# Performance work log

Hardware: AMD Instinct MI355X
Metric: run time of the kernel (lower is better)

## Reference

```python
import jax, jax.numpy as jnp
import numpy as np

N = 100_000   # nodes
E = 3_200_000 # edges
G = 512       # graphs in batch
H = 64        # hidden dim
C = 7         # num classes


def setup_inputs() -> dict:
    key = jax.random.key(0)
    ks = jax.random.split(key, 8)
    x = jax.random.normal(ks[0], (N, 1), dtype=jnp.float32)
    edge_index = jax.random.randint(ks[1], (2, E), 0, N, dtype=jnp.int32)
    batch = jnp.sort(jax.random.randint(ks[2], (N,), 0, G, dtype=jnp.int32))
    W1 = jax.random.normal(ks[3], (1, H), dtype=jnp.float32) / np.sqrt(1.0)
    b1 = jnp.zeros((H,), jnp.float32)
    W2 = jax.random.normal(ks[4], (H, H), dtype=jnp.float32) / np.sqrt(H)
    b2 = jnp.zeros((H,), jnp.float32)
    fW1 = jax.random.normal(ks[5], (H, 32), dtype=jnp.float32) / np.sqrt(H)
    fb1 = jnp.zeros((32,), jnp.float32)
    fW2 = jax.random.normal(ks[6], (32, C), dtype=jnp.float32) / np.sqrt(32.0)
    fb2 = jnp.zeros((C,), jnp.float32)
    return {"x": x, "edge_index": edge_index, "batch": batch,
            "W1": W1, "b1": b1, "W2": W2, "b2": b2,
            "fW1": fW1, "fb1": fb1, "fW2": fW2, "fb2": fb2}


def reference(x, edge_index, batch, W1, b1, W2, b2, fW1, fb1, fW2, fb2):
    # GCNConv with self-loops and symmetric normalization (PyG defaults).
    src, dst = edge_index[0], edge_index[1]
    loop = jnp.arange(N, dtype=src.dtype)
    s = jnp.concatenate([src, loop])  # [E+N]
    d = jnp.concatenate([dst, loop])
    deg = jax.ops.segment_sum(jnp.ones(s.shape, jnp.float32), d, num_segments=N)
    dis = jnp.where(deg > 0, jax.lax.rsqrt(jnp.maximum(deg, 1.0)), 0.0)
    norm = dis[s] * dis[d]  # [E+N]

    def gcn(h, W, b):
        h = h @ W                                   # [N, out]
        msg = norm[:, None] * h[s]                  # gather + scale
        return jax.ops.segment_sum(msg, d, num_segments=N) + b

    # Dropout is identity in eval/reference mode.
    h = jax.nn.relu(gcn(x, W1, b1))
    h = jax.nn.relu(gcn(h, W2, b2))

    # global_mean_pool over graph assignment `batch`
    cnt = jax.ops.segment_sum(jnp.ones((N,), jnp.float32), batch, num_segments=G)
    pooled = jax.ops.segment_sum(h, batch, num_segments=G) / jnp.maximum(cnt, 1.0)[:, None]

    h = jax.nn.relu(pooled @ fW1 + fb1)
    return h @ fW2 + fb2  # [G, C] logits
```

## Files before the change

### kernel.cpp

```cpp
#include <hip/hip_runtime.h>

#define N_NODES 100000
#define N_EDGES 3200000
#define G_GRAPHS 512
#define HDIM 64
#define CBSH 11
#define CBN 2048
#define NCB ((N_NODES + CBN - 1) / CBN)
#define EPW 4096
#define NWG ((N_EDGES + EPW - 1) / EPW)
#define EPT (EPW / 256)
#define SPL 16
#define WPS ((NWG + SPL - 1) / SPL)
#define MAXROWS 25

__global__ __launch_bounds__(256) void kprep(const float* __restrict__ W1,
                                             const float* __restrict__ b1,
                                             const float* __restrict__ W2,
                                             float* __restrict__ dt, int* __restrict__ meta,
                                             float* __restrict__ pw1, float* __restrict__ pb1,
                                             int* __restrict__ pdidx,
                                             float* __restrict__ w2p, float* __restrict__ tabs) {
    __shared__ float ts[HDIM], srt[HDIM];
    __shared__ int isnew[HDIM], rr[HDIM], kpermS[HDIM], rankS[HDIM];
    __shared__ int ndS;
    int tid = threadIdx.x;
    if (tid < HDIM) {
        float w1 = W1[tid], bb = b1[tid];
        ts[tid] = (w1 != 0.f) ? (-bb / w1) : -1e30f;
    }
    __syncthreads();
    if (tid < HDIM) {
        float tj = ts[tid];
        int r = 0;
        for (int i = 0; i < HDIM; ++i) {
            float ti = ts[i];
            if (ti < tj || (ti == tj && i < tid)) r++;
        }
        rr[tid] = r;
        srt[r] = tj;
        kpermS[r] = tid;
    }
    __syncthreads();
    if (tid < HDIM) {
        int r = rr[tid];
        isnew[r] = (r == 0) || (srt[r] != srt[r - 1]);
    }
    __syncthreads();
    if (tid < HDIM) {
        int r = rr[tid];
        int didx = 0;
        for (int q = 0; q <= r; ++q) didx += isnew[q];
        didx -= 1;
        rankS[tid] = didx;
        if (blockIdx.x == 0 && isnew[r]) dt[didx] = srt[r];
    }
    if (tid == 0) {
        int nd = 0;
        for (int q = 0; q < HDIM; ++q) nd += isnew[q];
        ndS = nd;
        if (blockIdx.x == 0) {
            int nw = 0;
            for (int q = 0; q < HDIM; ++q) nw |= (b1[q] != 0.f) ? 1 : 0;
            meta[0] = nd; meta[1] = nw;
        }
    }
    __syncthreads();
    int nd = ndS;
    if (blockIdx.x == 0 && tid < HDIM) {
        int pj = kpermS[tid];
        pw1[tid] = W1[pj]; pb1[tid] = b1[pj]; pdidx[tid] = rankS[pj];
    }
    int i = blockIdx.x * 256 + tid;
    if (i < HDIM * HDIM) {
        int r = i >> 6, j = i & 63;
        w2p[i] = W2[kpermS[r] * HDIM + j];
    }
    if (nd <= 6 && i < (1 + 4 * nd) * HDIM) {
        int r = i >> 6, j = i & 63;
        float acc = 0.f;
        if (r == 0) {
            for (int jj = 0; jj < HDIM; ++jj)
                if (W1[jj] == 0.f) acc += fmaxf(b1[jj], 0.f) * W2[jj * HDIM + j];
        } else {
            int q = (r - 1) >> 2, c = (r - 1) & 3;
            for (int jj = 0; jj < HDIM; ++jj) {
                if (rankS[jj] != q) continue;
                float w1 = W1[jj], bb = b1[jj];
                float wr = W2[jj * HDIM + j];
                if      (c == 0 && w1 > 0.f) acc += w1 * wr;
                else if (c == 1 && w1 < 0.f) acc += w1 * wr;
                else if (c == 2 && w1 > 0.f) acc += bb * wr;
                else if (c == 3 && w1 < 0.f) acc += bb * wr;
            }
        }
        tabs[i] = acc;
    }
}

__global__ void kzero(int* __restrict__ deg, float* __restrict__ q,
                      float* __restrict__ pool, int* __restrict__ cnt,
                      float* __restrict__ histA, float* __restrict__ histW) {
    size_t tid = (size_t)blockIdx.x * blockDim.x + threadIdx.x;
    size_t stride = (size_t)gridDim.x * blockDim.x;
    for (size_t i = tid; i < N_NODES; i += stride) { deg[i] = 0; q[i] = 0.f; }
    for (size_t i = tid; i < G_GRAPHS * HDIM; i += stride) pool[i] = 0.f;
    for (size_t i = tid; i < G_GRAPHS; i += stride) cnt[i] = 0;
    size_t nh = (size_t)7 * N_NODES;
    for (size_t i = tid; i < nh; i += stride) { histA[i] = 0.f; histW[i] = 0.f; }
}

__global__ __launch_bounds__(256) void kB2(const int* __restrict__ src,
                                           const int* __restrict__ dst,
                                           unsigned* __restrict__ sorted,
                                           int* __restrict__ wgcnt,
                                           int* __restrict__ wgpre) {
    __shared__ int hist[NCB];
    __shared__ int basep[NCB];
    __shared__ unsigned sbuf[EPW];
    int tid = threadIdx.x;
    int w = blockIdx.x;
    int e0 = w * EPW;
    int ecnt = min(EPW, N_EDGES - e0);
    if (tid < NCB) hist[tid] = 0;
    __syncthreads();
    int dreg[EPT], sreg[EPT];
    const uint4* dst4 = reinterpret_cast<const uint4*>(dst + e0);
    const uint4* src4 = reinterpret_cast<const uint4*>(src + e0);
    #pragma unroll
    for (int t = 0; t < EPT / 4; ++t) {
        int v = t * 256 + tid;
        if (v * 4 < ecnt) {
            uint4 dv = dst4[v];
            uint4 sv = src4[v];
            int base = v * 4;
            int d0 = (int)dv.x, d1 = (int)dv.y, d2 = (int)dv.z, d3 = (int)dv.w;
            dreg[t*4+0] = (base+0 < ecnt) ? d0 : -1;
            dreg[t*4+1] = (base+1 < ecnt) ? d1 : -1;
            dreg[t*4+2] = (base+2 < ecnt) ? d2 : -1;
            dreg[t*4+3] = (base+3 < ecnt) ? d3 : -1;
            sreg[t*4+0] = (int)sv.x; sreg[t*4+1] = (int)sv.y;
            sreg[t*4+2] = (int)sv.z; sreg[t*4+3] = (int)sv.w;
            #pragma unroll
            for (int k = 0; k < 4; ++k)
                if (dreg[t*4+k] >= 0) atomicAdd(&hist[dreg[t*4+k] >> CBSH], 1);
        } else {
            dreg[t*4+0] = dreg[t*4+1] = dreg[t*4+2] = dreg[t*4+3] = -1;
        }
    }
    __syncthreads();
    if (tid < 64) {
        int h = (tid < NCB) ? hist[tid] : 0;
        int v = h;
        #pragma unroll
        for (int off = 1; off < 64; off <<= 1) {
            int uu = __shfl_up(v, off, 64);
            if (tid >= off) v += uu;
        }
        if (tid < NCB) {
            basep[tid] = v - h;
            wgcnt[w * NCB + tid] = h;
            wgpre[w * NCB + tid] = v - h;
        }
    }
    __syncthreads();
    #pragma unroll
    for (int t = 0; t < EPT; ++t) {
        int d = dreg[t];
        if (d >= 0) {
            int b = d >> CBSH;
            int pos = atomicAdd(&basep[b], 1);
            sbuf[pos] = ((unsigned)sreg[t] << CBSH) | (unsigned)(d & (CBN - 1));
        }
    }
    __syncthreads();
    uint4* out4 = reinterpret_cast<uint4*>(sorted + e0);
    const uint4* sb4 = reinterpret_cast<const uint4*>(sbuf);
    int nv4 = ecnt >> 2;
    for (int i = tid; i < nv4; i += 256) out4[i] = sb4[i];
    for (int i = (nv4 << 2) + tid; i < ecnt; i += 256) sorted[e0 + i] = sbuf[i];
}

#define FOR_RUNS(BODY)                                                        \
    {                                                                         \
        int wv = tid >> 6, ln = tid & 63;                                     \
        int w0 = sp * WPS, w1e = min(w0 + WPS, NWG);                          \
        for (int w = w0 + wv; w < w1e; w += 4) {                              \
            int st = w * EPW + wgpre[w * NCB + b];                            \
            int cb = wgcnt[w * NCB + b];                                      \
            for (int i = ln; i < cb; i += 64) { unsigned ww = sorted[st + i]; BODY } \
        }                                                                     \
    }

__global__ __launch_bounds__(256) void kdeg2(const unsigned* __restrict__ sorted,
                                             const int* __restrict__ wgcnt,
                                             const int* __restrict__ wgpre,
                                             int* __restrict__ deg) {
    __shared__ int dcnt[CBN];
    int b = blockIdx.x / SPL, sp = blockIdx.x % SPL, tid = threadIdx.x;
    for (int i = tid; i < CBN; i += 256) dcnt[i] = 0;
    __syncthreads();
    FOR_RUNS( atomicAdd(&dcnt[ww & (CBN - 1)], 1); )
    __syncthreads();
    int nb = b * CBN;
    for (int i = tid; i < CBN; i += 256) {
        int c = dcnt[i];
        if (c && nb + i < N_NODES) atomicAdd(&deg[nb + i], c);
    }
}

__global__ void k2_dis(const int* __restrict__ deg, const float* __restrict__ x,
                       float* __restrict__ dis, float* __restrict__ u) {
    int n = blockIdx.x * blockDim.x + threadIdx.x;
    if (n < N_NODES) {
        float d = rsqrtf((float)(deg[n] + 1));
        dis[n] = d;
        u[n] = d * x[n];
    }
}

__global__ __launch_bounds__(256) void kq3(const unsigned* __restrict__ sorted,
                                           const int* __restrict__ wgcnt,
                                           const int* __restrict__ wgpre,
                                           const float* __restrict__ u,
                                           float* __restrict__ q) {
    __shared__ float qL[CBN];
    int b = blockIdx.x / SPL, sp = blockIdx.x % SPL, tid = threadIdx.x;
    for (int i = tid; i < CBN; i += 256) qL[i] = 0.f;
    __syncthreads();
    FOR_RUNS( atomicAdd(&qL[ww & (CBN - 1)], u[ww >> CBSH]); )
    __syncthreads();
    int nb = b * CBN;
    for (int i = tid; i < CBN; i += 256) {
        float v = qL[i];
        if (v != 0.f && nb + i < N_NODES) atomicAdd(&q[nb + i], v);
    }
}

__global__ void k3b(const int* __restrict__ deg, const float* __restrict__ x,
                    const float* __restrict__ dis, const float* __restrict__ q,
                    float2* __restrict__ ad) {
    int n = blockIdx.x * blockDim.x + threadIdx.x;
    if (n < N_NODES) {
        float d = dis[n];
        ad[n] = make_float2(d * q[n] + x[n] / (float)(deg[n] + 1), d);
    }
}

template<int LO, int HI, int PLANES>
__global__ __launch_bounds__(256) void khist3t(const unsigned* __restrict__ sorted,
                                               const int* __restrict__ wgcnt,
                                               const int* __restrict__ wgpre,
                                               const float2* __restrict__ ad,
                                               const float* __restrict__ dt,
                                               const int* __restrict__ meta,
                                               float* __restrict__ histA,
                                               float* __restrict__ histW) {
    __shared__ float bA[PLANES * CBN];
    __shared__ float dtS[8];
    int nd = meta[0], needW = meta[1];
    if (nd < LO || nd > HI) return;
    int b = blockIdx.x / SPL, sp = blockIdx.x % SPL, tid = threadIdx.x;
    if (tid < 8) dtS[tid] = (tid < nd) ? dt[tid] : 3.4e38f;
    int nb = b * CBN;
    int nparts = 1 + (needW ? 1 : 0);
    for (int part = 0; part < nparts; ++part) {
        for (int i = tid; i < (nd + 1) * CBN; i += 256) bA[i] = 0.f;
        __syncthreads();
        FOR_RUNS(
            float2 t = ad[ww >> CBSH];
            float a = t.x;
            int k = 0;
            _Pragma("unroll")
            for (int qq = 0; qq < HI; ++qq) k += (dtS[qq] < a) ? 1 : 0;
            atomicAdd(&bA[k * CBN + (ww & (CBN - 1))], part ? t.y : t.y * a);
        )
        __syncthreads();
        float* H = part ? histW : histA;
        for (int k = 0; k <= nd; ++k)
            for (int i = tid; i < CBN; i += 256) {
                float v = bA[k * CBN + i];
                if (v != 0.f && nb + i < N_NODES)
                    atomicAdd(&H[(size_t)k * N_NODES + nb + i], v);
            }
        __syncthreads();
    }
}

__global__ __launch_bounds__(256) void knode(
        const float* __restrict__ histA, const float* __restrict__ histW,
        const int* __restrict__ meta, const float* __restrict__ dt,
        const float* __restrict__ tabs,
        const float* __restrict__ pw1, const float* __restrict__ pb1,
        const float* __restrict__ w2p,
        const float2* __restrict__ ad, const float* __restrict__ b2,
        const int* __restrict__ batch,
        const unsigned* __restrict__ sorted, const int* __restrict__ wgcnt,
        const int* __restrict__ wgpre,
        float* __restrict__ pool, int* __restrict__ cnt) {
    __shared__ float h2s[HDIM * 65];
    __shared__ float tabL[MAXROWS * HDIM];
    __shared__ float dtS[8];
    int tid = threadIdx.x;
    int nl = tid & 63, cg = tid >> 6;
    int n0 = blockIdx.x * 64;
    int nvalid = min(64, N_NODES - n0);
    int n = n0 + min(nl, nvalid - 1);
    int nd = meta[0], needW = meta[1];
    float2 adn = ad[n];
    float a = adn.x, d = adn.y;
    int c16 = cg * 16;

    if (nd <= 6) {
        int nrows = 1 + 4 * nd;
        for (int i = tid; i < nrows * HDIM; i += 256) tabL[i] = tabs[i];
        if (tid < nd) dtS[tid] = dt[tid];
        __syncthreads();
        float TA = 0.f, TW = 0.f;
        for (int bq = 0; bq <= nd; ++bq) {
            TA += histA[(size_t)bq * N_NODES + n];
            if (needW) TW += histW[(size_t)bq * N_NODES + n];
        }
        int k = 0;
        for (int q = 0; q < nd; ++q) k += (dtS[q] < a) ? 1 : 0;
        float z[16];
        #pragma unroll
        for (int t = 0; t < 16; ++t) z[t] = b2[c16 + t];
        float d2 = d * d;
        float cC = d * TW + d2;
        #pragma unroll
        for (int t = 0; t < 16; ++t) z[t] += cC * tabL[c16 + t];
        float run = 0.f, runW = 0.f;
        for (int q = 0; q < nd; ++q) {
            run += histA[(size_t)q * N_NODES + n];
            if (needW) runW += histW[(size_t)q * N_NODES + n];
            bool act = (q < k);
            float cWp = d * (TA - run) + (act ? d2 * a : 0.f);
            float cWm = d * run + (act ? 0.f : d2 * a);
            float cBp = d * (TW - runW) + (act ? d2 : 0.f);
            float cBm = d * runW + (act ? 0.f : d2);
            int base = (1 + 4 * q) * HDIM + c16;
            #pragma unroll
            for (int t = 0; t < 16; ++t)
                z[t] += cWp * tabL[base + t] + cWm * tabL[base + HDIM + t]
                      + cBp * tabL[base + 2 * HDIM + t] + cBm * tabL[base + 3 * HDIM + t];
        }
        #pragma unroll
        for (int t = 0; t < 16; ++t) h2s[nl * 65 + c16 + t] = fmaxf(z[t], 0.f);
    } else {
        float areg[HDIM];
        #pragma unroll
        for (int jj = 0; jj < HDIM; ++jj) areg[jj] = 0.f;
        int b = n >> CBSH;
        int myld = n & (CBN - 1);
        for (int w = 0; w < NWG; ++w) {
            int st = w * EPW + wgpre[w * NCB + b];
            int cb = wgcnt[w * NCB + b];
            for (int i = 0; i < cb; ++i) {
                unsigned ww = sorted[st + i];
                if ((int)(ww & (CBN - 1)) == myld) {
                    float2 t = ad[ww >> CBSH];
                    #pragma unroll
                    for (int jj = 0; jj < HDIM; ++jj)
                        areg[jj] += t.y * fmaxf(t.x * pw1[jj] + pb1[jj], 0.f);
                }
            }
        }
        #pragma unroll
        for (int jj = 0; jj < HDIM; ++jj)
            areg[jj] = d * areg[jj] + d * d * fmaxf(a * pw1[jj] + pb1[jj], 0.f);
        float z[16];
        #pragma unroll
        for (int t = 0; t < 16; ++t) z[t] = b2[c16 + t];
        for (int jj = 0; jj < HDIM; ++jj) {
            float av = areg[jj];
            #pragma unroll
            for (int t = 0; t < 16; ++t) z[t] += av * w2p[jj * HDIM + c16 + t];
        }
        #pragma unroll
        for (int t = 0; t < 16; ++t) h2s[nl * 65 + c16 + t] = fmaxf(z[t], 0.f);
    }

    __syncthreads();
    int i0 = cg * 16, i1 = min(i0 + 16, nvalid);
    float accP = 0.f; int gcur = -1, runC = 0;
    for (int i = i0; i < i1; ++i) {
        int g = batch[n0 + i];
        float v = h2s[i * 65 + nl];
        if (g != gcur) {
            if (gcur >= 0) {
                atomicAdd(&pool[(size_t)gcur * HDIM + nl], accP);
                if (nl == 0) atomicAdd(&cnt[gcur], runC);
            }
            gcur = g; accP = 0.f; runC = 0;
        }
        accP += v; ++runC;
    }
    if (gcur >= 0) {
        atomicAdd(&pool[(size_t)gcur * HDIM + nl], accP);
        if (nl == 0) atomicAdd(&cnt[gcur], runC);
    }
}

__global__ void k7_mlp(const float* __restrict__ pool, const int* __restrict__ cnt,
                       const float* __restrict__ fW1, const float* __restrict__ fb1,
                       const float* __restrict__ fW2, const float* __restrict__ fb2,
                       float* __restrict__ out) {
    __shared__ float p[HDIM];
    __shared__ float tt[32];
    int g = blockIdx.x;
    int tid = threadIdx.x;
    float c = fmaxf((float)cnt[g], 1.f);
    p[tid] = pool[g * HDIM + tid] / c;
    __syncthreads();
    if (tid < 32) {
        float acc = fb1[tid];
        #pragma unroll
        for (int j = 0; j < HDIM; ++j) acc += p[j] * fW1[j * 32 + tid];
        tt[tid] = fmaxf(acc, 0.f);
    }
    __syncthreads();
    if (tid < 7) {
        float acc = fb2[tid];
        #pragma unroll
        for (int i = 0; i < 32; ++i) acc += tt[i] * fW2[i * 7 + tid];
        out[g * 7 + tid] = acc;
    }
}

__global__ void kf1_deg(const int* __restrict__ dst, int* __restrict__ deg) {
    int e = blockIdx.x * blockDim.x + threadIdx.x;
    if (e < N_EDGES) atomicAdd(&deg[dst[e]], 1);
}
__global__ void kf2_dis(const int* __restrict__ deg, const float* __restrict__ x,
                        float* __restrict__ dis, float* __restrict__ agg1) {
    int n = blockIdx.x * blockDim.x + threadIdx.x;
    if (n < N_NODES) {
        float d = (float)(deg[n] + 1);
        dis[n] = rsqrtf(d);
        agg1[n] = x[n] / d;
    }
}
__global__ void kf3_agg1(const int* __restrict__ src, const int* __restrict__ dst,
                         const float* __restrict__ dis, const float* __restrict__ x,
                         float* __restrict__ agg1) {
    int e = blockIdx.x * blockDim.x + threadIdx.x;
    if (e < N_EDGES) {
        int s = src[e], d = dst[e];
        atomicAdd(&agg1[d], dis[s] * dis[d] * x[s]);
    }
}
__global__ void kf4_agg2init(const float* __restrict__ agg1, const float* __restrict__ dis,
                             const float* __restrict__ W1, const float* __restrict__ b1,
                             float* __restrict__ agg2) {
    int i = blockIdx.x * blockDim.x + threadIdx.x;
    if (i < N_NODES * HDIM) {
        int n = i >> 6, j = i & 63;
        float h = fmaxf(agg1[n] * W1[j] + b1[j], 0.f);
        float r = dis[n];
        agg2[i] = r * r * h;
    }
}
__global__ void kf5_edge(const int* __restrict__ src, const int* __restrict__ dst,
                         const float* __restrict__ dis, const float* __restrict__ agg1,
                         const float* __restrict__ W1, const float* __restrict__ b1,
                         float* __restrict__ agg2) {
    int t = blockIdx.x * blockDim.x + threadIdx.x;
    int e = t >> 6, j = t & 63;
    if (e < N_EDGES) {
        int s = src[e], d = dst[e];
        float w = dis[s] * dis[d];
        float h = fmaxf(agg1[s] * W1[j] + b1[j], 0.f);
        atomicAdd(&agg2[d * HDIM + j], w * h);
    }
}
__global__ void kf6_pool(const float* __restrict__ agg2, const float* __restrict__ W2,
                         const float* __restrict__ b2, const int* __restrict__ batch,
                         float* __restrict__ pool, int* __restrict__ cnt) {
    __shared__ float w2s[HDIM * HDIM];
    int tid = threadIdx.x;
    for (int i = tid; i < HDIM * HDIM; i += blockDim.x) w2s[i] = W2[i];
    __syncthreads();
    int lane = tid & 63, wid = tid >> 6;
    int nwaves = gridDim.x * 4;
    for (int n = blockIdx.x * 4 + wid; n < N_NODES; n += nwaves) {
        float av  = agg2[n * HDIM + lane];
        float acc = b2[lane];
        #pragma unroll
        for (int k = 0; k < HDIM; ++k)
            acc += __shfl(av, k, 64) * w2s[k * HDIM + lane];
        acc = fmaxf(acc, 0.f);
        int g = batch[n];
        atomicAdd(&pool[g * HDIM + lane], acc);
        if (lane == 0) atomicAdd(&cnt[g], 1);
    }
}

extern "C" void kernel_launch(void* const* d_in, const int* in_sizes, int n_in,
                              void* d_out, int out_size, void* d_ws, size_t ws_size,
                              hipStream_t stream) {
    const float* x    = (const float*)d_in[0];
    const int*   ei   = (const int*)  d_in[1];
    const int*   batch= (const int*)  d_in[2];
    const float* W1   = (const float*)d_in[3];
    const float* b1   = (const float*)d_in[4];
    const float* W2   = (const float*)d_in[5];
    const float* b2   = (const float*)d_in[6];
    const float* fW1  = (const float*)d_in[7];
    const float* fb1  = (const float*)d_in[8];
    const float* fW2  = (const float*)d_in[9];
    const float* fb2  = (const float*)d_in[10];
    const int* src = ei;
    const int* dst = ei + N_EDGES;
    float* out = (float*)d_out;

    size_t off = 0;
    auto take = [&](size_t bytes) { size_t o = off; off = (off + bytes + 255) & ~(size_t)255; return o; };
    char* base = (char*)d_ws;
    int*     deg   = (int*)     (base + take((size_t)N_NODES * 4));
    float*   pool  = (float*)   (base + take((size_t)G_GRAPHS * HDIM * 4));
    int*     cnt   = (int*)     (base + take((size_t)G_GRAPHS * 4));
    float*   dis   = (float*)   (base + take((size_t)N_NODES * 4));
    float*   u     = (float*)   (base + take((size_t)N_NODES * 4));
    float*   q     = (float*)   (base + take((size_t)N_NODES * 4));
    float2*  ad    = (float2*)  (base + take((size_t)N_NODES * 8));
    float*   dt    = (float*)   (base + take(HDIM * 4));
    int*     meta  = (int*)     (base + take(64));
    float*   pw1   = (float*)   (base + take(HDIM * 4));
    float*   pb1   = (float*)   (base + take(HDIM * 4));
    int*     pdidx = (int*)     (base + take(HDIM * 4));
    float*   w2p   = (float*)   (base + take(HDIM * HDIM * 4));
    float*   tabs  = (float*)   (base + take((size_t)MAXROWS * HDIM * 4));
    int*     wgcnt = (int*)     (base + take((size_t)NWG * NCB * 4));
    int*     wgpre = (int*)     (base + take((size_t)NWG * NCB * 4));
    size_t sorted_off = off;
    unsigned* sorted = (unsigned*)(base + take((size_t)N_EDGES * 4));
    float*   histA = (float*)   (base + take((size_t)7 * N_NODES * 4));
    float*   histW = (float*)   (base + take((size_t)7 * N_NODES * 4));
    size_t need_fast = off;

    if (ws_size >= need_fast) {
        kprep <<<16, 256, 0, stream>>>(W1, b1, W2, dt, meta, pw1, pb1, pdidx, w2p, tabs);
        kzero <<<1024, 256, 0, stream>>>(deg, q, pool, cnt, histA, histW);
        kB2   <<<NWG, 256, 0, stream>>>(src, dst, sorted, wgcnt, wgpre);
        kdeg2 <<<NCB * SPL, 256, 0, stream>>>(sorted, wgcnt, wgpre, deg);
        k2_dis<<<(N_NODES + 255) / 256, 256, 0, stream>>>(deg, x, dis, u);
        kq3   <<<NCB * SPL, 256, 0, stream>>>(sorted, wgcnt, wgpre, u, q);
        k3b   <<<(N_NODES + 255) / 256, 256, 0, stream>>>(deg, x, dis, q, ad);
        khist3t<0, 1, 2><<<NCB * SPL, 256, 0, stream>>>(sorted, wgcnt, wgpre, ad, dt, meta, histA, histW);
        khist3t<2, 6, 7><<<NCB * SPL, 256, 0, stream>>>(sorted, wgcnt, wgpre, ad, dt, meta, histA, histW);
        knode <<<(N_NODES + 63) / 64, 256, 0, stream>>>(histA, histW, meta, dt, tabs,
                                                        pw1, pb1, w2p, ad, b2, batch,
                                                        sorted, wgcnt, wgpre, pool, cnt);
        k7_mlp<<<G_GRAPHS, 64, 0, stream>>>(pool, cnt, fW1, fb1, fW2, fb2, out);
    } else {
        float* agg1 = u;
        float* agg2 = (float*)(base + sorted_off);
        hipMemsetAsync(deg, 0, (size_t)N_NODES * 4, stream);
        hipMemsetAsync(pool, 0, (size_t)G_GRAPHS * HDIM * 4 + 1024, stream);
        kf1_deg<<<(N_EDGES + 255) / 256, 256, 0, stream>>>(dst, deg);
        kf2_dis<<<(N_NODES + 255) / 256, 256, 0, stream>>>(deg, x, dis, agg1);
        kf3_agg1<<<(N_EDGES + 255) / 256, 256, 0, stream>>>(src, dst, dis, x, agg1);
        kf4_agg2init<<<(N_NODES * HDIM + 255) / 256, 256, 0, stream>>>(agg1, dis, W1, b1, agg2);
        int k5_blocks = (int)(((long long)N_EDGES * HDIM + 255) / 256);
        kf5_edge<<<k5_blocks, 256, 0, stream>>>(src, dst, dis, agg1, W1, b1, agg2);
        kf6_pool<<<2048, 256, 0, stream>>>(agg2, W2, b2, batch, pool, cnt);
        k7_mlp<<<G_GRAPHS, 64, 0, stream>>>(pool, cnt, fW1, fb1, fW2, fb2, out);
    }
}
```

Measured before the change: 149.7 us.

## Fuse prep/zero kernels, widen scatter blocks, split node kernel by path

```diff
diff --git a/kernel.cpp b/kernel.cpp
--- a/kernel.cpp
+++ b/kernel.cpp
@@ -10,104 +10,105 @@
 #define EPW 4096
 #define NWG ((N_EDGES + EPW - 1) / EPW)
 #define EPT (EPW / 256)
-#define SPL 16
+#define SPL 8
+#define RTHR 512
 #define WPS ((NWG + SPL - 1) / SPL)
 #define MAXROWS 25
 
-__global__ __launch_bounds__(256) void kprep(const float* __restrict__ W1,
-                                             const float* __restrict__ b1,
-                                             const float* __restrict__ W2,
-                                             float* __restrict__ dt, int* __restrict__ meta,
-                                             float* __restrict__ pw1, float* __restrict__ pb1,
-                                             int* __restrict__ pdidx,
-                                             float* __restrict__ w2p, float* __restrict__ tabs) {
-    __shared__ float ts[HDIM], srt[HDIM];
-    __shared__ int isnew[HDIM], rr[HDIM], kpermS[HDIM], rankS[HDIM];
-    __shared__ int ndS;
+__global__ __launch_bounds__(256) void kzp(const float* __restrict__ W1,
+                                           const float* __restrict__ b1,
+                                           const float* __restrict__ W2,
+                                           float* __restrict__ dt, int* __restrict__ meta,
+                                           float* __restrict__ pw1, float* __restrict__ pb1,
+                                           int* __restrict__ pdidx,
+                                           float* __restrict__ w2p, float* __restrict__ tabs,
+                                           int* __restrict__ deg, float* __restrict__ q,
+                                           float* __restrict__ pool, int* __restrict__ cnt,
+                                           float* __restrict__ histA, float* __restrict__ histW) {
     int tid = threadIdx.x;
-    if (tid < HDIM) {
-        float w1 = W1[tid], bb = b1[tid];
-        ts[tid] = (w1 != 0.f) ? (-bb / w1) : -1e30f;
-    }
-    __syncthreads();
-    if (tid < HDIM) {
-        float tj = ts[tid];
-        int r = 0;
-        for (int i = 0; i < HDIM; ++i) {
-            float ti = ts[i];
-            if (ti < tj || (ti == tj && i < tid)) r++;
-        }
-        rr[tid] = r;
-        srt[r] = tj;
-        kpermS[r] = tid;
-    }
-    __syncthreads();
-    if (tid < HDIM) {
-        int r = rr[tid];
-        isnew[r] = (r == 0) || (srt[r] != srt[r - 1]);
-    }
-    __syncthreads();
-    if (tid < HDIM) {
-        int r = rr[tid];
-        int didx = 0;
-        for (int q = 0; q <= r; ++q) didx += isnew[q];
-        didx -= 1;
-        rankS[tid] = didx;
-        if (blockIdx.x == 0 && isnew[r]) dt[didx] = srt[r];
-    }
-    if (tid == 0) {
-        int nd = 0;
-        for (int q = 0; q < HDIM; ++q) nd += isnew[q];
-        ndS = nd;
-        if (blockIdx.x == 0) {
-            int nw = 0;
-            for (int q = 0; q < HDIM; ++q) nw |= (b1[q] != 0.f) ? 1 : 0;
-            meta[0] = nd; meta[1] = nw;
-        }
-    }
-    __syncthreads();
-    int nd = ndS;
-    if (blockIdx.x == 0 && tid < HDIM) {
-        int pj = kpermS[tid];
-        pw1[tid] = W1[pj]; pb1[tid] = b1[pj]; pdidx[tid] = rankS[pj];
-    }
-    int i = blockIdx.x * 256 + tid;
-    if (i < HDIM * HDIM) {
-        int r = i >> 6, j = i & 63;
-        w2p[i] = W2[kpermS[r] * HDIM + j];
-    }
-    if (nd <= 6 && i < (1 + 4 * nd) * HDIM) {
-        int r = i >> 6, j = i & 63;
-        float acc = 0.f;
-        if (r == 0) {
-            for (int jj = 0; jj < HDIM; ++jj)
-                if (W1[jj] == 0.f) acc += fmaxf(b1[jj], 0.f) * W2[jj * HDIM + j];
-        } else {
-            int q = (r - 1) >> 2, c = (r - 1) & 3;
-            for (int jj = 0; jj < HDIM; ++jj) {
-                if (rankS[jj] != q) continue;
-                float w1 = W1[jj], bb = b1[jj];
-                float wr = W2[jj * HDIM + j];
-                if      (c == 0 && w1 > 0.f) acc += w1 * wr;
-                else if (c == 1 && w1 < 0.f) acc += w1 * wr;
-                else if (c == 2 && w1 > 0.f) acc += bb * wr;
-                else if (c == 3 && w1 < 0.f) acc += bb * wr;
+    if (blockIdx.x < 16) {
+        __shared__ float ts[HDIM], srt[HDIM];
+        __shared__ int isnew[HDIM], rr[HDIM], kpermS[HDIM], rankS[HDIM];
+        __shared__ int ndS;
+        if (tid < HDIM) {
+            float w1 = W1[tid], bb = b1[tid];
+            ts[tid] = (w1 != 0.f) ? (-bb / w1) : -1e30f;
+        }
+        __syncthreads();
+        if (tid < HDIM) {
+            float tj = ts[tid];
+            int r = 0;
+            for (int i = 0; i < HDIM; ++i) {
+                float ti = ts[i];
+                if (ti < tj || (ti == tj && i < tid)) r++;
             }
-        }
-        tabs[i] = acc;
-    }
-}
-
-__global__ void kzero(int* __restrict__ deg, float* __restrict__ q,
-                      float* __restrict__ pool, int* __restrict__ cnt,
-                      float* __restrict__ histA, float* __restrict__ histW) {
-    size_t tid = (size_t)blockIdx.x * blockDim.x + threadIdx.x;
+            rr[tid] = r;
+            srt[r] = tj;
+            kpermS[r] = tid;
+        }
+        __syncthreads();
+        if (tid < HDIM) {
+            int r = rr[tid];
+            isnew[r] = (r == 0) || (srt[r] != srt[r - 1]);
+        }
+        __syncthreads();
+        if (tid < HDIM) {
+            int r = rr[tid];
+            int didx = 0;
+            for (int qq = 0; qq <= r; ++qq) didx += isnew[qq];
+            didx -= 1;
+            rankS[tid] = didx;
+            if (blockIdx.x == 0 && isnew[r]) dt[didx] = srt[r];
+        }
+        if (tid == 0) {
+            int nd = 0;
+            for (int qq = 0; qq < HDIM; ++qq) nd += isnew[qq];
+            ndS = nd;
+            if (blockIdx.x == 0) {
+                int nw = 0;
+                for (int qq = 0; qq < HDIM; ++qq) nw |= (b1[qq] != 0.f) ? 1 : 0;
+                meta[0] = nd; meta[1] = nw;
+            }
+        }
+        __syncthreads();
+        int nd = ndS;
+        if (blockIdx.x == 0 && tid < HDIM) {
+            int pj = kpermS[tid];
+            pw1[tid] = W1[pj]; pb1[tid] = b1[pj]; pdidx[tid] = rankS[pj];
+        }
+        int i = blockIdx.x * 256 + tid;
+        if (i < HDIM * HDIM) {
+            int r = i >> 6, j = i & 63;
+            w2p[i] = W2[kpermS[r] * HDIM + j];
+        }
+        if (nd <= 6 && i < (1 + 4 * nd) * HDIM) {
+            int r = i >> 6, j = i & 63;
+            float acc = 0.f;
+            if (r == 0) {
+                for (int jj = 0; jj < HDIM; ++jj)
+                    if (W1[jj] == 0.f) acc += fmaxf(b1[jj], 0.f) * W2[jj * HDIM + j];
+            } else {
+                int qq = (r - 1) >> 2, c = (r - 1) & 3;
+                for (int jj = 0; jj < HDIM; ++jj) {
+                    if (rankS[jj] != qq) continue;
+                    float w1 = W1[jj], bb = b1[jj];
+                    float wr = W2[jj * HDIM + j];
+                    if      (c == 0 && w1 > 0.f) acc += w1 * wr;
+                    else if (c == 1 && w1 < 0.f) acc += w1 * wr;
+                    else if (c == 2 && w1 > 0.f) acc += bb * wr;
+                    else if (c == 3 && w1 < 0.f) acc += bb * wr;
+                }
+            }
+            tabs[i] = acc;
+        }
+    }
+    size_t gtid = (size_t)blockIdx.x * blockDim.x + threadIdx.x;
     size_t stride = (size_t)gridDim.x * blockDim.x;
-    for (size_t i = tid; i < N_NODES; i += stride) { deg[i] = 0; q[i] = 0.f; }
-    for (size_t i = tid; i < G_GRAPHS * HDIM; i += stride) pool[i] = 0.f;
-    for (size_t i = tid; i < G_GRAPHS; i += stride) cnt[i] = 0;
+    for (size_t i = gtid; i < N_NODES; i += stride) { deg[i] = 0; q[i] = 0.f; }
+    for (size_t i = gtid; i < G_GRAPHS * HDIM; i += stride) pool[i] = 0.f;
+    for (size_t i = gtid; i < G_GRAPHS; i += stride) cnt[i] = 0;
     size_t nh = (size_t)7 * N_NODES;
-    for (size_t i = tid; i < nh; i += stride) { histA[i] = 0.f; histW[i] = 0.f; }
+    for (size_t i = gtid; i < nh; i += stride) { histA[i] = 0.f; histW[i] = 0.f; }
 }
 
 __global__ __launch_bounds__(256) void kB2(const int* __restrict__ src,
@@ -134,11 +135,10 @@
             uint4 dv = dst4[v];
             uint4 sv = src4[v];
             int base = v * 4;
-            int d0 = (int)dv.x, d1 = (int)dv.y, d2 = (int)dv.z, d3 = (int)dv.w;
-            dreg[t*4+0] = (base+0 < ecnt) ? d0 : -1;
-            dreg[t*4+1] = (base+1 < ecnt) ? d1 : -1;
-            dreg[t*4+2] = (base+2 < ecnt) ? d2 : -1;
-            dreg[t*4+3] = (base+3 < ecnt) ? d3 : -1;
+            dreg[t*4+0] = (base+0 < ecnt) ? (int)dv.x : -1;
+            dreg[t*4+1] = (base+1 < ecnt) ? (int)dv.y : -1;
+            dreg[t*4+2] = (base+2 < ecnt) ? (int)dv.z : -1;
+            dreg[t*4+3] = (base+3 < ecnt) ? (int)dv.w : -1;
             sreg[t*4+0] = (int)sv.x; sreg[t*4+1] = (int)sv.y;
             sreg[t*4+2] = (int)sv.z; sreg[t*4+3] = (int)sv.w;
             #pragma unroll
@@ -185,25 +185,25 @@
     {                                                                         \
         int wv = tid >> 6, ln = tid & 63;                                     \
         int w0 = sp * WPS, w1e = min(w0 + WPS, NWG);                          \
-        for (int w = w0 + wv; w < w1e; w += 4) {                              \
+        for (int w = w0 + wv; w < w1e; w += (RTHR / 64)) {                    \
             int st = w * EPW + wgpre[w * NCB + b];                            \
             int cb = wgcnt[w * NCB + b];                                      \
             for (int i = ln; i < cb; i += 64) { unsigned ww = sorted[st + i]; BODY } \
         }                                                                     \
     }
 
-__global__ __launch_bounds__(256) void kdeg2(const unsigned* __restrict__ sorted,
-                                             const int* __restrict__ wgcnt,
-                                             const int* __restrict__ wgpre,
-                                             int* __restrict__ deg) {
+__global__ __launch_bounds__(RTHR) void kdeg2(const unsigned* __restrict__ sorted,
+                                              const int* __restrict__ wgcnt,
+                                              const int* __restrict__ wgpre,
+                                              int* __restrict__ deg) {
     __shared__ int dcnt[CBN];
     int b = blockIdx.x / SPL, sp = blockIdx.x % SPL, tid = threadIdx.x;
-    for (int i = tid; i < CBN; i += 256) dcnt[i] = 0;
+    for (int i = tid; i < CBN; i += RTHR) dcnt[i] = 0;
     __syncthreads();
     FOR_RUNS( atomicAdd(&dcnt[ww & (CBN - 1)], 1); )
     __syncthreads();
     int nb = b * CBN;
-    for (int i = tid; i < CBN; i += 256) {
+    for (int i = tid; i < CBN; i += RTHR) {
         int c = dcnt[i];
         if (c && nb + i < N_NODES) atomicAdd(&deg[nb + i], c);
     }
@@ -219,19 +219,19 @@
     }
 }
 
-__global__ __launch_bounds__(256) void kq3(const unsigned* __restrict__ sorted,
-                                           const int* __restrict__ wgcnt,
-                                           const int* __restrict__ wgpre,
-                                           const float* __restrict__ u,
-                                           float* __restrict__ q) {
+__global__ __launch_bounds__(RTHR) void kq3(const unsigned* __restrict__ sorted,
+                                            const int* __restrict__ wgcnt,
+                                            const int* __restrict__ wgpre,
+                                            const float* __restrict__ u,
+                                            float* __restrict__ q) {
     __shared__ float qL[CBN];
     int b = blockIdx.x / SPL, sp = blockIdx.x % SPL, tid = threadIdx.x;
-    for (int i = tid; i < CBN; i += 256) qL[i] = 0.f;
+    for (int i = tid; i < CBN; i += RTHR) qL[i] = 0.f;
     __syncthreads();
     FOR_RUNS( atomicAdd(&qL[ww & (CBN - 1)], u[ww >> CBSH]); )
     __syncthreads();
     int nb = b * CBN;
-    for (int i = tid; i < CBN; i += 256) {
+    for (int i = tid; i < CBN; i += RTHR) {
         float v = qL[i];
         if (v != 0.f && nb + i < N_NODES) atomicAdd(&q[nb + i], v);
     }
@@ -248,14 +248,14 @@
 }
 
 template<int LO, int HI, int PLANES>
-__global__ __launch_bounds__(256) void khist3t(const unsigned* __restrict__ sorted,
-                                               const int* __restrict__ wgcnt,
-                                               const int* __restrict__ wgpre,
-                                               const float2* __restrict__ ad,
-                                               const float* __restrict__ dt,
-                                               const int* __restrict__ meta,
-                                               float* __restrict__ histA,
-                                               float* __restrict__ histW) {
+__global__ __launch_bounds__(RTHR) void khist3t(const unsigned* __restrict__ sorted,
+                                                const int* __restrict__ wgcnt,
+                                                const int* __restrict__ wgpre,
+                                                const float2* __restrict__ ad,
+                                                const float* __restrict__ dt,
+                                                const int* __restrict__ meta,
+                                                float* __restrict__ histA,
+                                                float* __restrict__ histW) {
     __shared__ float bA[PLANES * CBN];
     __shared__ float dtS[8];
     int nd = meta[0], needW = meta[1];
@@ -265,7 +265,7 @@
     int nb = b * CBN;
     int nparts = 1 + (needW ? 1 : 0);
     for (int part = 0; part < nparts; ++part) {
-        for (int i = tid; i < (nd + 1) * CBN; i += 256) bA[i] = 0.f;
+        for (int i = tid; i < (nd + 1) * CBN; i += RTHR) bA[i] = 0.f;
         __syncthreads();
         FOR_RUNS(
             float2 t = ad[ww >> CBSH];
@@ -278,7 +278,7 @@
         __syncthreads();
         float* H = part ? histW : histA;
         for (int k = 0; k <= nd; ++k)
-            for (int i = tid; i < CBN; i += 256) {
+            for (int i = tid; i < CBN; i += RTHR) {
                 float v = bA[k * CBN + i];
                 if (v != 0.f && nb + i < N_NODES)
                     atomicAdd(&H[(size_t)k * N_NODES + nb + i], v);
@@ -287,10 +287,86 @@
     }
 }
 
-__global__ __launch_bounds__(256) void knode(
+__global__ __launch_bounds__(256) void knode_fast(
         const float* __restrict__ histA, const float* __restrict__ histW,
         const int* __restrict__ meta, const float* __restrict__ dt,
         const float* __restrict__ tabs,
+        const float2* __restrict__ ad, const float* __restrict__ b2,
+        const int* __restrict__ batch,
+        float* __restrict__ pool, int* __restrict__ cnt) {
+    __shared__ float h2s[HDIM * 65];
+    __shared__ float tabL[MAXROWS * HDIM];
+    __shared__ float dtS[8];
+    int nd = meta[0], needW = meta[1];
+    if (nd > 6) return;
+    int tid = threadIdx.x;
+    int nl = tid & 63, cg = tid >> 6;
+    int n0 = blockIdx.x * 64;
+    int nvalid = min(64, N_NODES - n0);
+    int n = n0 + min(nl, nvalid - 1);
+    float2 adn = ad[n];
+    float a = adn.x, d = adn.y;
+    int c16 = cg * 16;
+
+    int nrows = 1 + 4 * nd;
+    for (int i = tid; i < nrows * HDIM; i += 256) tabL[i] = tabs[i];
+    if (tid < nd) dtS[tid] = dt[tid];
+    __syncthreads();
+    float TA = 0.f, TW = 0.f;
+    for (int bq = 0; bq <= nd; ++bq) {
+        TA += histA[(size_t)bq * N_NODES + n];
+        if (needW) TW += histW[(size_t)bq * N_NODES + n];
+    }
+    int k = 0;
+    for (int q = 0; q < nd; ++q) k += (dtS[q] < a) ? 1 : 0;
+    float z[16];
+    #pragma unroll
+    for (int t = 0; t < 16; ++t) z[t] = b2[c16 + t];
+    float d2 = d * d;
+    float cC = d * TW + d2;
+    #pragma unroll
+    for (int t = 0; t < 16; ++t) z[t] += cC * tabL[c16 + t];
+    float run = 0.f, runW = 0.f;
+    for (int q = 0; q < nd; ++q) {
+        run += histA[(size_t)q * N_NODES + n];
+        if (needW) runW += histW[(size_t)q * N_NODES + n];
+        bool act = (q < k);
+        float cWp = d * (TA - run) + (act ? d2 * a : 0.f);
+        float cWm = d * run + (act ? 0.f : d2 * a);
+        float cBp = d * (TW - runW) + (act ? d2 : 0.f);
+        float cBm = d * runW + (act ? 0.f : d2);
+        int base = (1 + 4 * q) * HDIM + c16;
+        #pragma unroll
+        for (int t = 0; t < 16; ++t)
+            z[t] += cWp * tabL[base + t] + cWm * tabL[base + HDIM + t]
+                  + cBp * tabL[base + 2 * HDIM + t] + cBm * tabL[base + 3 * HDIM + t];
+    }
+    #pragma unroll
+    for (int t = 0; t < 16; ++t) h2s[nl * 65 + c16 + t] = fmaxf(z[t], 0.f);
+
+    __syncthreads();
+    int i0 = cg * 16, i1 = min(i0 + 16, nvalid);
+    float accP = 0.f; int gcur = -1, runC = 0;
+    for (int i = i0; i < i1; ++i) {
+        int g = batch[n0 + i];
+        float v = h2s[i * 65 + nl];
+        if (g != gcur) {
+            if (gcur >= 0) {
+                atomicAdd(&pool[(size_t)gcur * HDIM + nl], accP);
+                if (nl == 0) atomicAdd(&cnt[gcur], runC);
+            }
+            gcur = g; accP = 0.f; runC = 0;
+        }
+        accP += v; ++runC;
+    }
+    if (gcur >= 0) {
+        atomicAdd(&pool[(size_t)gcur * HDIM + nl], accP);
+        if (nl == 0) atomicAdd(&cnt[gcur], runC);
+    }
+}
+
+__global__ __launch_bounds__(256) void knode_gen(
+        const int* __restrict__ meta,
         const float* __restrict__ pw1, const float* __restrict__ pb1,
         const float* __restrict__ w2p,
         const float2* __restrict__ ad, const float* __restrict__ b2,
@@ -298,88 +374,48 @@
         const unsigned* __restrict__ sorted, const int* __restrict__ wgcnt,
         const int* __restrict__ wgpre,
         float* __restrict__ pool, int* __restrict__ cnt) {
+    int nd = meta[0];
+    if (nd <= 6) return;
     __shared__ float h2s[HDIM * 65];
-    __shared__ float tabL[MAXROWS * HDIM];
-    __shared__ float dtS[8];
     int tid = threadIdx.x;
     int nl = tid & 63, cg = tid >> 6;
     int n0 = blockIdx.x * 64;
     int nvalid = min(64, N_NODES - n0);
     int n = n0 + min(nl, nvalid - 1);
-    int nd = meta[0], needW = meta[1];
     float2 adn = ad[n];
     float a = adn.x, d = adn.y;
     int c16 = cg * 16;
-
-    if (nd <= 6) {
-        int nrows = 1 + 4 * nd;
-        for (int i = tid; i < nrows * HDIM; i += 256) tabL[i] = tabs[i];
-        if (tid < nd) dtS[tid] = dt[tid];
-        __syncthreads();
-        float TA = 0.f, TW = 0.f;
-        for (int bq = 0; bq <= nd; ++bq) {
-            TA += histA[(size_t)bq * N_NODES + n];
-            if (needW) TW += histW[(size_t)bq * N_NODES + n];
-        }
-        int k = 0;
-        for (int q = 0; q < nd; ++q) k += (dtS[q] < a) ? 1 : 0;
-        float z[16];
+    float areg[HDIM];
+    #pragma unroll
+    for (int jj = 0; jj < HDIM; ++jj) areg[jj] = 0.f;
+    int b = n >> CBSH;
+    int myld = n & (CBN - 1);
+    for (int w = 0; w < NWG; ++w) {
+        int st = w * EPW + wgpre[w * NCB + b];
+        int cb = wgcnt[w * NCB + b];
+        for (int i = 0; i < cb; ++i) {
+            unsigned ww = sorted[st + i];
+            if ((int)(ww & (CBN - 1)) == myld) {
+                float2 t = ad[ww >> CBSH];
+                #pragma unroll
+                for (int jj = 0; jj < HDIM; ++jj)
+                    areg[jj] += t.y * fmaxf(t.x * pw1[jj] + pb1[jj], 0.f);
+            }
+        }
+    }
+    #pragma unroll
+    for (int jj = 0; jj < HDIM; ++jj)
+        areg[jj] = d * areg[jj] + d * d * fmaxf(a * pw1[jj] + pb1[jj], 0.f);
+    float z[16];
+    #pragma unroll
+    for (int t = 0; t < 16; ++t) z[t] = b2[c16 + t];
+    for (int jj = 0; jj < HDIM; ++jj) {
+        float av = areg[jj];
         #pragma unroll
-        for (int t = 0; t < 16; ++t) z[t] = b2[c16 + t];
-        float d2 = d * d;
-        float cC = d * TW + d2;
-        #pragma unroll
-        for (int t = 0; t < 16; ++t) z[t] += cC * tabL[c16 + t];
-        float run = 0.f, runW = 0.f;
-        for (int q = 0; q < nd; ++q) {
-            run += histA[(size_t)q * N_NODES + n];
-            if (needW) runW += histW[(size_t)q * N_NODES + n];
-            bool act = (q < k);
-            float cWp = d * (TA - run) + (act ? d2 * a : 0.f);
-            float cWm = d * run + (act ? 0.f : d2 * a);
-            float cBp = d * (TW - runW) + (act ? d2 : 0.f);
-            float cBm = d * runW + (act ? 0.f : d2);
-            int base = (1 + 4 * q) * HDIM + c16;
-            #pragma unroll
-            for (int t = 0; t < 16; ++t)
-                z[t] += cWp * tabL[base + t] + cWm * tabL[base + HDIM + t]
-                      + cBp * tabL[base + 2 * HDIM + t] + cBm * tabL[base + 3 * HDIM + t];
-        }
-        #pragma unroll
-        for (int t = 0; t < 16; ++t) h2s[nl * 65 + c16 + t] = fmaxf(z[t], 0.f);
-    } else {
-        float areg[HDIM];
-        #pragma unroll
-        for (int jj = 0; jj < HDIM; ++jj) areg[jj] = 0.f;
-        int b = n >> CBSH;
-        int myld = n & (CBN - 1);
-        for (int w = 0; w < NWG; ++w) {
-            int st = w * EPW + wgpre[w * NCB + b];
-            int cb = wgcnt[w * NCB + b];
-            for (int i = 0; i < cb; ++i) {
-                unsigned ww = sorted[st + i];
-                if ((int)(ww & (CBN - 1)) == myld) {
-                    float2 t = ad[ww >> CBSH];
-                    #pragma unroll
-                    for (int jj = 0; jj < HDIM; ++jj)
-                        areg[jj] += t.y * fmaxf(t.x * pw1[jj] + pb1[jj], 0.f);
-                }
-            }
-        }
-        #pragma unroll
-        for (int jj = 0; jj < HDIM; ++jj)
-            areg[jj] = d * areg[jj] + d * d * fmaxf(a * pw1[jj] + pb1[jj], 0.f);
-        float z[16];
-        #pragma unroll
-        for (int t = 0; t < 16; ++t) z[t] = b2[c16 + t];
-        for (int jj = 0; jj < HDIM; ++jj) {
-            float av = areg[jj];
-            #pragma unroll
-            for (int t = 0; t < 16; ++t) z[t] += av * w2p[jj * HDIM + c16 + t];
-        }
-        #pragma unroll
-        for (int t = 0; t < 16; ++t) h2s[nl * 65 + c16 + t] = fmaxf(z[t], 0.f);
-    }
+        for (int t = 0; t < 16; ++t) z[t] += av * w2p[jj * HDIM + c16 + t];
+    }
+    #pragma unroll
+    for (int t = 0; t < 16; ++t) h2s[nl * 65 + c16 + t] = fmaxf(z[t], 0.f);
 
     __syncthreads();
     int i0 = cg * 16, i1 = min(i0 + 16, nvalid);
@@ -540,18 +576,19 @@
     size_t need_fast = off;
 
     if (ws_size >= need_fast) {
-        kprep <<<16, 256, 0, stream>>>(W1, b1, W2, dt, meta, pw1, pb1, pdidx, w2p, tabs);
-        kzero <<<1024, 256, 0, stream>>>(deg, q, pool, cnt, histA, histW);
+        kzp   <<<1024, 256, 0, stream>>>(W1, b1, W2, dt, meta, pw1, pb1, pdidx, w2p, tabs,
+                                         deg, q, pool, cnt, histA, histW);
         kB2   <<<NWG, 256, 0, stream>>>(src, dst, sorted, wgcnt, wgpre);
-        kdeg2 <<<NCB * SPL, 256, 0, stream>>>(sorted, wgcnt, wgpre, deg);
+        kdeg2 <<<NCB * SPL, RTHR, 0, stream>>>(sorted, wgcnt, wgpre, deg);
         k2_dis<<<(N_NODES + 255) / 256, 256, 0, stream>>>(deg, x, dis, u);
-        kq3   <<<NCB * SPL, 256, 0, stream>>>(sorted, wgcnt, wgpre, u, q);
+        kq3   <<<NCB * SPL, RTHR, 0, stream>>>(sorted, wgcnt, wgpre, u, q);
         k3b   <<<(N_NODES + 255) / 256, 256, 0, stream>>>(deg, x, dis, q, ad);
-        khist3t<0, 1, 2><<<NCB * SPL, 256, 0, stream>>>(sorted, wgcnt, wgpre, ad, dt, meta, histA, histW);
-        khist3t<2, 6, 7><<<NCB * SPL, 256, 0, stream>>>(sorted, wgcnt, wgpre, ad, dt, meta, histA, histW);
-        knode <<<(N_NODES + 63) / 64, 256, 0, stream>>>(histA, histW, meta, dt, tabs,
-                                                        pw1, pb1, w2p, ad, b2, batch,
-                                                        sorted, wgcnt, wgpre, pool, cnt);
+        khist3t<0, 1, 2><<<NCB * SPL, RTHR, 0, stream>>>(sorted, wgcnt, wgpre, ad, dt, meta, histA, histW);
+        khist3t<2, 6, 7><<<NCB * SPL, RTHR, 0, stream>>>(sorted, wgcnt, wgpre, ad, dt, meta, histA, histW);
+        knode_fast<<<(N_NODES + 63) / 64, 256, 0, stream>>>(histA, histW, meta, dt, tabs,
+                                                            ad, b2, batch, pool, cnt);
+        knode_gen <<<(N_NODES + 63) / 64, 256, 0, stream>>>(meta, pw1, pb1, w2p, ad, b2, batch,
+                                                            sorted, wgcnt, wgpre, pool, cnt);
         k7_mlp<<<G_GRAPHS, 64, 0, stream>>>(pool, cnt, fW1, fb1, fW2, fb2, out);
     } else {
         float* agg1 = u;
```

Measured after the change: 135.1 us. 1.11x faster.
